# Optimization experiments

Hardware: AMD Instinct MI355X
Metric: run time of the kernel (lower is better)

## Reference

```python
import jax, jax.numpy as jnp
import numpy as np

K_ACTIVE = 32
MULTI_K = 64
AUX_K = 64
DEAD_THRESH = 256


def setup_inputs() -> dict:
    key = jax.random.key(0)
    ks = jax.random.split(key, 4)
    B, D, M = 4096, 1024, 16384
    x = jax.random.normal(ks[0], (B, D), dtype=jnp.float32)
    enc_w = jax.random.normal(ks[1], (M, D), dtype=jnp.float32) / np.sqrt(D)
    dec_w = jax.random.normal(ks[2], (D, M), dtype=jnp.float32) / np.sqrt(M)
    input_bias = jnp.zeros((D,), dtype=jnp.float32)
    neuron_bias = jnp.zeros((M,), dtype=jnp.float32)
    steps = jax.random.randint(ks[3], (M,), 0, 512).astype(jnp.int64)
    return {"x": x, "enc_w": enc_w, "dec_w": dec_w,
            "input_bias": input_bias, "neuron_bias": neuron_bias, "steps": steps}


def reference(x, enc_w, dec_w, input_bias, neuron_bias, steps):
    # encode: center, linear (no bias), add neuron bias, relu
    x_cent = x - input_bias                                   # [B, D]
    pre_act = x_cent @ enc_w.T + neuron_bias                  # [B, M]
    acts = jax.nn.relu(pre_act)
    B, M = acts.shape

    # training path: global batch-wide top-(K*B) across flattened activations
    flat = acts.reshape(-1)                                   # [B*M]
    topk_vals, topk_idx = jax.lax.top_k(flat, K_ACTIVE * B)
    activ = jnp.zeros_like(flat).at[topk_idx].set(topk_vals).reshape(B, M)

    # multi-k branch: per-row top-k on pre-activations, relu, scatter, decode
    mvals, midx = jax.lax.top_k(pre_act, MULTI_K)             # [B, MULTI_K]
    mvals = jax.nn.relu(mvals)
    rows = jnp.arange(B)[:, None]
    multik_activ = jnp.zeros_like(pre_act).at[rows, midx].set(mvals)
    multik_recon = multik_activ @ dec_w.T + input_bias        # [B, D]

    # main reconstruction
    recon = activ @ dec_w.T + input_bias                      # [B, D]

    # dead-neuron bookkeeping + aux top-k over dead neurons
    steps = steps + 1
    active = activ.sum(axis=0) > 0                            # [M]
    steps = jnp.where(active, jnp.zeros_like(steps), steps)
    dead_mask = (steps > DEAD_THRESH).astype(pre_act.dtype)   # [M]
    dead_pre = pre_act * dead_mask                            # [B, M]
    aux_vals, aux_idx = jax.lax.top_k(dead_pre, AUX_K)        # [B, AUX_K]
    aux_vals = jax.nn.relu(aux_vals)

    return recon, activ, multik_recon, aux_vals, aux_idx
```

## Files before the change

### kernel.cpp

```cpp
#include <hip/hip_runtime.h>

#define K_ACTIVE 32
#define MULTI_K 64
#define AUX_K 64
#define DEAD_THRESH 256
#define BUF_CAP 262144u
#define SORT_CAP 4096

typedef unsigned int u32;
typedef unsigned long long u64;
typedef unsigned short ushort_t;
typedef __bf16 bf16x8 __attribute__((ext_vector_type(8)));
typedef float f32x4 __attribute__((ext_vector_type(4)));

__device__ __forceinline__ u32 fmap_signed_bits(u32 u) {
  return (u & 0x80000000u) ? ~u : (u | 0x80000000u);
}

__device__ __forceinline__ u32 bf16_rne(float f) {
  u32 u = __float_as_uint(f);
  return (u + 0x7FFFu + ((u >> 16) & 1u)) >> 16;
}

__device__ __forceinline__ void gload16(const void* g, void* s) {
  __builtin_amdgcn_global_load_lds(
      (const __attribute__((address_space(1))) void*)g,
      (__attribute__((address_space(3))) void*)s, 16, 0, 0);
}

__global__ void transpose_k(const float* __restrict__ in, float* __restrict__ out, int D, int M) {
  __shared__ float tile[32][33];
  const int bx = blockIdx.x * 32;
  const int by = blockIdx.y * 32;
  const int tx = threadIdx.x, ty = threadIdx.y;
  #pragma unroll
  for (int i = 0; i < 32; i += 8)
    tile[ty + i][tx] = in[(size_t)(by + ty + i) * M + bx + tx];
  __syncthreads();
  #pragma unroll
  for (int i = 0; i < 32; i += 8)
    out[(size_t)(bx + ty + i) * D + by + tx] = tile[tx][ty + i];
}

__global__ void convA_k(const float* __restrict__ X, const float* __restrict__ IB,
                        ushort_t* __restrict__ AH, ushort_t* __restrict__ AL, int D) {
  const int idx = blockIdx.x * 256 + threadIdx.x;
  const int row = idx >> 7;
  const int dpos = (idx & 127) << 3;
  const float4* xr = reinterpret_cast<const float4*>(X + (size_t)row * D + dpos);
  const float4* br = reinterpret_cast<const float4*>(IB + dpos);
  float4 x0 = xr[0], x1 = xr[1], b0 = br[0], b1 = br[1];
  float c[8] = {x0.x - b0.x, x0.y - b0.y, x0.z - b0.z, x0.w - b0.w,
                x1.x - b1.x, x1.y - b1.y, x1.z - b1.z, x1.w - b1.w};
  u32 hw[4], lw[4];
  #pragma unroll
  for (int j = 0; j < 4; ++j) {
    u32 h0 = bf16_rne(c[2 * j]), h1 = bf16_rne(c[2 * j + 1]);
    float r0 = c[2 * j] - __uint_as_float(h0 << 16);
    float r1 = c[2 * j + 1] - __uint_as_float(h1 << 16);
    hw[j] = h0 | (h1 << 16);
    lw[j] = bf16_rne(r0) | (bf16_rne(r1) << 16);
  }
  reinterpret_cast<uint4*>(AH)[idx] = make_uint4(hw[0], hw[1], hw[2], hw[3]);
  reinterpret_cast<uint4*>(AL)[idx] = make_uint4(lw[0], lw[1], lw[2], lw[3]);
}

__global__ void convW_k(const float* __restrict__ W,
                        ushort_t* __restrict__ WH, ushort_t* __restrict__ WL) {
  const int idx = blockIdx.x * 256 + threadIdx.x;
  const float4* wr = reinterpret_cast<const float4*>(W) + (size_t)idx * 2;
  float4 x0 = wr[0], x1 = wr[1];
  float c[8] = {x0.x, x0.y, x0.z, x0.w, x1.x, x1.y, x1.z, x1.w};
  u32 hw[4], lw[4];
  #pragma unroll
  for (int j = 0; j < 4; ++j) {
    u32 h0 = bf16_rne(c[2 * j]), h1 = bf16_rne(c[2 * j + 1]);
    float r0 = c[2 * j] - __uint_as_float(h0 << 16);
    float r1 = c[2 * j + 1] - __uint_as_float(h1 << 16);
    hw[j] = h0 | (h1 << 16);
    lw[j] = bf16_rne(r0) | (bf16_rne(r1) << 16);
  }
  reinterpret_cast<uint4*>(WH)[idx] = make_uint4(hw[0], hw[1], hw[2], hw[3]);
  reinterpret_cast<uint4*>(WL)[idx] = make_uint4(lw[0], lw[1], lw[2], lw[3]);
}

__global__ __launch_bounds__(256) void gemm_mfma(
    const ushort_t* __restrict__ AH, const ushort_t* __restrict__ AL,
    const ushort_t* __restrict__ WH, const ushort_t* __restrict__ WL,
    const float* __restrict__ NB, float* __restrict__ OUT,
    u32* __restrict__ GH, int M) {
  extern __shared__ char smem[];
  ushort_t* sA = (ushort_t*)smem;
  ushort_t* sB = (ushort_t*)(smem + 16384);
  const int tid = threadIdx.x;
  const int wave = tid >> 6, lane = tid & 63;
  const int bm = blockIdx.y * 128, bn = blockIdx.x * 128;
  const int wm = wave & 1, wn = wave >> 1;

  f32x4 acc[4][4];
  #pragma unroll
  for (int i = 0; i < 4; ++i)
    #pragma unroll
    for (int j = 0; j < 4; ++j) acc[i][j] = (f32x4){0.f, 0.f, 0.f, 0.f};

  int rowA[4], cbS[4];
  #pragma unroll
  for (int r = 0; r < 4; ++r) {
    int o = ((wave << 2) + r) * 1024 + lane * 16;
    int row = o >> 7;
    int cb = o & 127;
    rowA[r] = row;
    cbS[r] = cb ^ ((row & 7) << 4);
  }
  const int cl = lane & 15, kg = lane >> 4;

  for (int kt = 0; kt < 48; ++kt) {
    const int ph = kt >> 4;
    const size_t kb = (size_t)((kt & 15) << 6) * 2;
    const ushort_t* Asrc = (ph == 1) ? AL : AH;
    const ushort_t* Bsrc = (ph == 2) ? WL : WH;
    #pragma unroll
    for (int r = 0; r < 4; ++r) {
      gload16((const char*)Asrc + ((size_t)(bm + rowA[r]) * 2048 + kb + cbS[r]),
              (char*)sA + (((wave << 2) + r) << 10));
      gload16((const char*)Bsrc + ((size_t)(bn + rowA[r]) * 2048 + kb + cbS[r]),
              (char*)sB + (((wave << 2) + r) << 10));
    }
    __syncthreads();
    #pragma unroll
    for (int ks = 0; ks < 2; ++ks) {
      const int kbyte = ks * 64 + kg * 16;
      bf16x8 af[4], bfr[4];
      #pragma unroll
      for (int mi = 0; mi < 4; ++mi) {
        const int rA = wm * 64 + mi * 16 + cl;
        af[mi] = *reinterpret_cast<const bf16x8*>(
            (const char*)sA + rA * 128 + (kbyte ^ ((rA & 7) << 4)));
      }
      #pragma unroll
      for (int ni = 0; ni < 4; ++ni) {
        const int rB = wn * 64 + ni * 16 + cl;
        bfr[ni] = *reinterpret_cast<const bf16x8*>(
            (const char*)sB + rB * 128 + (kbyte ^ ((rB & 7) << 4)));
      }
      #pragma unroll
      for (int mi = 0; mi < 4; ++mi)
        #pragma unroll
        for (int ni = 0; ni < 4; ++ni)
          acc[mi][ni] = __builtin_amdgcn_mfma_f32_16x16x32_bf16(af[mi], bfr[ni], acc[mi][ni], 0, 0, 0);
    }
    __syncthreads();
  }

  u32* eh = (u32*)smem;
  for (int i = tid; i < 8192; i += 256) eh[i] = 0;
  __syncthreads();
  const int rg = lane >> 4;
  const int rb = (lane & 3) * 2048;
  #pragma unroll
  for (int ni = 0; ni < 4; ++ni) {
    const int col = bn + wn * 64 + ni * 16 + cl;
    const float nbv = NB[col];
    #pragma unroll
    for (int mi = 0; mi < 4; ++mi) {
      const int row0 = bm + wm * 64 + mi * 16 + rg * 4;
      #pragma unroll
      for (int r = 0; r < 4; ++r) {
        const float val = acc[mi][ni][r] + nbv;
        OUT[(size_t)(row0 + r) * M + col] = val;
        const float a = (val > 0.f) ? val : 0.f;
        atomicAdd(&eh[rb + (__float_as_uint(a) >> 21)], 1u);
      }
    }
  }
  __syncthreads();
  for (int i = tid; i < 2048; i += 256) {
    u32 s = eh[i] + eh[2048 + i] + eh[4096 + i] + eh[6144 + i];
    if (s) atomicAdd(&GH[i], s);
  }
}

__global__ void scan_k(const u32* __restrict__ H, u32* __restrict__ PRM, u32 K, int phase) {
  __shared__ u32 suf[256];
  const int t = threadIdx.x;
  u32 h[8], ls[8];
  #pragma unroll
  for (int j = 0; j < 8; ++j) h[j] = H[t * 8 + j];
  u32 run = 0;
  #pragma unroll
  for (int j = 7; j >= 0; --j) { run += h[j]; ls[j] = run; }
  suf[t] = run;
  __syncthreads();
  for (int off = 1; off < 256; off <<= 1) {
    u32 v = (t + off < 256) ? suf[t + off] : 0u;
    __syncthreads();
    suf[t] += v;
    __syncthreads();
  }
  const u32 rightOf = (t < 255) ? suf[t + 1] : 0u;
  const u32 base = (phase == 2) ? PRM[1] : 0u;
  #pragma unroll
  for (int j = 0; j < 8; ++j) {
    u32 Sb = base + rightOf + ls[j];
    u32 Sb1 = base + rightOf + ((j < 7) ? ls[j + 1] : 0u);
    if (Sb >= K && Sb1 < K) {
      int b = t * 8 + j;
      if (phase == 1) { PRM[0] = (u32)b; PRM[1] = Sb1; }
      else { PRM[2] = (PRM[0] << 11) | (u32)b; PRM[3] = K - Sb1; }
    }
  }
}

__global__ void hist2_k(const float4* __restrict__ P4, size_t N4, const u32* __restrict__ PRM, u32* __restrict__ GH) {
  const u32 b1 = PRM[0];
  const size_t step = (size_t)gridDim.x * blockDim.x;
  for (size_t i = (size_t)blockIdx.x * blockDim.x + threadIdx.x; i < N4; i += step) {
    float4 vv = P4[i];
    float va[4] = {vv.x, vv.y, vv.z, vv.w};
    #pragma unroll
    for (int c = 0; c < 4; ++c) {
      float a = (va[c] > 0.f) ? va[c] : 0.f;
      u32 u = __float_as_uint(a);
      if ((u >> 21) == b1) atomicAdd(&GH[(u >> 10) & 2047u], 1u);
    }
  }
}

__global__ void collect_k(const float4* __restrict__ P4, size_t N4, u32* __restrict__ PRM,
                          float* __restrict__ BV, u32* __restrict__ BI,
                          u32* __restrict__ CF, int M) {
  const u32 pc = PRM[2];
  const size_t step = (size_t)gridDim.x * blockDim.x;
  for (size_t i = (size_t)blockIdx.x * blockDim.x + threadIdx.x; i < N4; i += step) {
    float4 vv = P4[i];
    float va[4] = {vv.x, vv.y, vv.z, vv.w};
    #pragma unroll
    for (int c = 0; c < 4; ++c) {
      float a = (va[c] > 0.f) ? va[c] : 0.f;
      u32 u = __float_as_uint(a);
      u32 bin = u >> 10;
      if (bin == pc) {
        u32 pos = atomicAdd(&PRM[8], 1u);
        if (pos < BUF_CAP) { BV[pos] = a; BI[pos] = (u32)(i * 4 + c); }
      } else if (bin > pc) {
        if (a > 0.f) CF[(u32)((i * 4 + c) % (size_t)M)] = 1u;
      }
    }
  }
}

__global__ void sortmark_k(u32* __restrict__ PRM, const float* __restrict__ BV, const u32* __restrict__ BI,
                           float* __restrict__ SV, u32* __restrict__ SI, u32* __restrict__ CF, int M) {
  __shared__ u64 keys[SORT_CAP];
  const int tid = threadIdx.x;
  u32 nb = PRM[8]; if (nb > SORT_CAP) nb = SORT_CAP;
  const u32 krem = PRM[3];
  if (nb == 0) { if (tid == 0) PRM[5] = 0; return; }
  u32 np = 1; while (np < nb) np <<= 1;
  for (u32 i = tid; i < np; i += 256)
    keys[i] = (i < nb) ? ((((u64)__float_as_uint(BV[i])) << 32) | (u64)(0xFFFFFFFFu - BI[i])) : 0ull;
  __syncthreads();
  for (u32 k = 2; k <= np; k <<= 1) {
    for (u32 j = k >> 1; j > 0; j >>= 1) {
      for (u32 i = tid; i < np; i += 256) {
        u32 ixj = i ^ j;
        if (ixj > i) {
          u64 a = keys[i], b = keys[ixj];
          bool up = ((i & k) == 0);
          if (up ? (a < b) : (a > b)) { keys[i] = b; keys[ixj] = a; }
        }
      }
      __syncthreads();
    }
  }
  u32 nsel = krem < nb ? krem : nb;
  for (u32 t = tid; t < nsel; t += 256) {
    u64 kk = keys[t];
    u32 flat = 0xFFFFFFFFu - (u32)(kk & 0xFFFFFFFFull);
    float val = __uint_as_float((u32)(kk >> 32));
    SI[t] = flat; SV[t] = val;
    if (val > 0.f) CF[flat % (u32)M] = 1u;
  }
  if (tid == 0) PRM[5] = nsel;
}

__global__ void dead_k(const u32* __restrict__ CF, const int* __restrict__ ST,
                       u32* __restrict__ DW, int M) {
  int w = blockIdx.x * blockDim.x + threadIdx.x;
  if (w >= M / 32) return;
  u32 bits = 0;
  for (int i = 0; i < 32; ++i) {
    int n = w * 32 + i;
    if (CF[n] == 0 && (ST[n] + 1) > DEAD_THRESH) bits |= (1u << i);
  }
  DW[w] = bits;
}

struct TopkSh {
  u32 hist[16 * 257];
  u32 wred[4];
  u32 prefix, need, scnt;
  int selN[64];
  float selV[64];
};

template<bool ZSKIP>
__device__ void row_topk64(const float (&v)[64], int tid, TopkSh* S) {
  const int lane = tid & 63, wid = tid >> 6;
  u32 zp = 0, zn = 0;
  if (ZSKIP) {
    #pragma unroll
    for (int j = 0; j < 64; ++j) {
      u32 ub = __float_as_uint(v[j]);
      zp += (ub == 0u);
      zn += (ub == 0x80000000u);
    }
    #pragma unroll
    for (int o = 32; o > 0; o >>= 1) { zp += __shfl_down(zp, o); zn += __shfl_down(zn, o); }
  }
  u32 pref = 0, need = 64;
  for (int p = 0; p < 4; ++p) {
    const int sh = 24 - 8 * p;
    for (int i = tid; i < 16 * 257; i += 256) S->hist[i] = 0;
    if (p == 0 && tid == 0) S->scnt = 0;
    __syncthreads();
    const int rb = (tid & 15) * 257;
    #pragma unroll
    for (int j = 0; j < 64; ++j) {
      u32 ub = __float_as_uint(v[j]);
      if (ZSKIP && ((ub << 1) == 0u)) continue;
      u32 mu = fmap_signed_bits(ub);
      if (p == 0 || (mu >> (sh + 8)) == pref)
        atomicAdd(&S->hist[rb + ((mu >> sh) & 255u)], 1u);
    }
    if (ZSKIP && lane == 0) {
      const u32 mup = 0x80000000u, mun = 0x7FFFFFFFu;
      if (zp && (p == 0 || (mup >> (sh + 8)) == pref))
        atomicAdd(&S->hist[wid * 257 + ((mup >> sh) & 255u)], zp);
      if (zn && (p == 0 || (mun >> (sh + 8)) == pref))
        atomicAdd(&S->hist[wid * 257 + ((mun >> sh) & 255u)], zn);
    }
    __syncthreads();
    u32 own = 0;
    #pragma unroll
    for (int r = 0; r < 16; ++r) own += S->hist[r * 257 + tid];
    u32 x = own;
    #pragma unroll
    for (int o = 1; o < 64; o <<= 1) {
      u32 y = __shfl_down(x, o);
      x += (lane + o < 64) ? y : 0u;
    }
    if (lane == 0) S->wred[wid] = x;
    __syncthreads();
    u32 Sb = x;
    for (int w = wid + 1; w < 4; ++w) Sb += S->wred[w];
    u32 below = Sb - own;
    if (Sb >= need && below < need) {
      S->prefix = (pref << 8) | (u32)tid;
      S->need = need - below;
    }
    __syncthreads();
    pref = S->prefix; need = S->need;
  }
  const u32 muc = pref, neq = need;
  u32 myeq = 0;
  #pragma unroll
  for (int j = 0; j < 64; ++j) {
    u32 mu = fmap_signed_bits(__float_as_uint(v[j]));
    if (mu > muc) {
      u32 pos = atomicAdd(&S->scnt, 1u);
      S->selN[pos] = tid * 64 + j;
      S->selV[pos] = v[j];
    } else if (mu == muc) ++myeq;
  }
  u32 xs = myeq;
  #pragma unroll
  for (int o = 1; o < 64; o <<= 1) {
    u32 y = __shfl_up(xs, o);
    xs += (lane >= o) ? y : 0u;
  }
  if (lane == 63) S->wred[wid] = xs;
  __syncthreads();
  u32 base = 0;
  for (int w = 0; w < wid; ++w) base += S->wred[w];
  u32 g = base + xs - myeq;
  const u32 a0 = S->scnt;
  #pragma unroll
  for (int j = 0; j < 64; ++j) {
    u32 mu = fmap_signed_bits(__float_as_uint(v[j]));
    if (mu == muc) {
      if (g < neq) { S->selN[a0 + g] = tid * 64 + j; S->selV[a0 + g] = v[j]; }
      ++g;
    }
  }
  __syncthreads();
}

__device__ __forceinline__ void load_row64(const float* rowp, float (&v)[64]) {
  #pragma unroll
  for (int j = 0; j < 16; ++j) {
    float4 t = reinterpret_cast<const float4*>(rowp)[j];
    v[4 * j + 0] = t.x; v[4 * j + 1] = t.y; v[4 * j + 2] = t.z; v[4 * j + 3] = t.w;
  }
}

__launch_bounds__(256, 2)
__global__ void rowk_multik(const float* __restrict__ PRE, const float* __restrict__ WT,
                            const float* __restrict__ IB, float* __restrict__ MR,
                            int M, int D) {
  __shared__ TopkSh S;
  const int b = blockIdx.x, tid = threadIdx.x;
  float v[64];
  load_row64(PRE + (size_t)b * M + tid * 64, v);
  row_topk64<false>(v, tid, &S);
  const int d0 = tid * 4;
  float4 acc = *reinterpret_cast<const float4*>(IB + d0);
  for (int i = 0; i < 64; ++i) {
    float w = S.selV[i];
    if (w > 0.f) {
      const float4 wv = *reinterpret_cast<const float4*>(WT + (size_t)S.selN[i] * D + d0);
      acc.x = fmaf(w, wv.x, acc.x); acc.y = fmaf(w, wv.y, acc.y);
      acc.z = fmaf(w, wv.z, acc.z); acc.w = fmaf(w, wv.w, acc.w);
    }
  }
  *reinterpret_cast<float4*>(MR + (size_t)b * D + d0) = acc;
}

__launch_bounds__(256, 2)
__global__ void rowk_aux(const float* __restrict__ PRE, const u32* __restrict__ DW,
                         float* __restrict__ AV, float* __restrict__ AI, int M) {
  __shared__ TopkSh S;
  __shared__ u64 skey[64];
  __shared__ int sN2[64];
  __shared__ float sV2[64];
  const int b = blockIdx.x, tid = threadIdx.x;
  float v[64];
  load_row64(PRE + (size_t)b * M + tid * 64, v);
  const u32 mw0 = DW[tid * 2], mw1 = DW[tid * 2 + 1];
  #pragma unroll
  for (int j = 0; j < 64; ++j) {
    u32 bit = ((j < 32 ? mw0 : mw1) >> (j & 31)) & 1u;
    v[j] = bit ? v[j] : (v[j] * 0.0f);
  }
  row_topk64<true>(v, tid, &S);
  if (tid < 64) {
    float vv = S.selV[tid];
    int col = S.selN[tid];
    u32 mu = fmap_signed_bits(__float_as_uint(vv));
    skey[tid] = (((u64)mu) << 32) | (u64)(0xFFFFFFFFu - (u32)col);
  }
  __syncthreads();
  if (tid < 64) {
    u64 mine = skey[tid];
    int rank = 0;
    for (int j = 0; j < 64; ++j) rank += (skey[j] > mine) ? 1 : 0;
    sN2[rank] = S.selN[tid]; sV2[rank] = S.selV[tid];
  }
  __syncthreads();
  if (tid < 64) {
    AV[(size_t)b * AUX_K + tid] = sV2[tid] > 0.f ? sV2[tid] : 0.f;
    AI[(size_t)b * AUX_K + tid] = (float)sN2[tid];
  }
}

__launch_bounds__(256, 2)
__global__ void rowk_scatter(float* __restrict__ ACT, const float* __restrict__ WT,
                             const float* __restrict__ IB, float* __restrict__ RC,
                             const u32* __restrict__ PRM, const float* __restrict__ SV,
                             const u32* __restrict__ SI, int M, int D) {
  __shared__ int lsN[2048]; __shared__ float lsV[2048];
  __shared__ int ovN[256]; __shared__ float ovV[256];
  __shared__ u32 ovc, lc;
  const int b = blockIdx.x, tid = threadIdx.x;
  float* rowp = ACT + (size_t)b * M + tid * 64;
  float v[64];
  load_row64(rowp, v);
  const u32 pc = PRM[2];
  #pragma unroll
  for (int j = 0; j < 64; ++j) {
    float a = (v[j] > 0.f) ? v[j] : 0.f;
    v[j] = ((__float_as_uint(a) >> 10) > pc) ? a : 0.f;
  }
  if (tid == 0) ovc = 0;
  __syncthreads();
  const u32 nbs = PRM[5];
  for (u32 t = tid; t < nbs; t += 256) {
    u32 flat = SI[t];
    if (flat / (u32)M == (u32)b) {
      u32 p = atomicAdd(&ovc, 1u);
      if (p < 256) { ovN[p] = (int)(flat % (u32)M); ovV[p] = SV[t]; }
    }
  }
  __syncthreads();
  const u32 no = ovc < 256u ? ovc : 256u;
  #pragma unroll
  for (int j = 0; j < 64; ++j) {
    const int col = tid * 64 + j;
    for (u32 i = 0; i < no; ++i) if (ovN[i] == col) v[j] = ovV[i];
  }
  #pragma unroll
  for (int j = 0; j < 16; ++j) {
    float4 t = make_float4(v[4 * j + 0], v[4 * j + 1], v[4 * j + 2], v[4 * j + 3]);
    reinterpret_cast<float4*>(rowp)[j] = t;
  }
  const int d0 = tid * 4;
  float4 acc = *reinterpret_cast<const float4*>(IB + d0);
  for (int cpart = 0; cpart < 8; ++cpart) {
    if (tid == 0) lc = 0;
    __syncthreads();
    if ((tid >> 5) == cpart) {
      #pragma unroll
      for (int j = 0; j < 64; ++j) {
        if (v[j] > 0.f) {
          u32 p = atomicAdd(&lc, 1u);
          lsN[p] = tid * 64 + j; lsV[p] = v[j];
        }
      }
    }
    __syncthreads();
    const u32 n = lc;
    for (u32 i = 0; i < n; ++i) {
      const float w = lsV[i];
      const float4 wv = *reinterpret_cast<const float4*>(WT + (size_t)lsN[i] * D + d0);
      acc.x = fmaf(w, wv.x, acc.x); acc.y = fmaf(w, wv.y, acc.y);
      acc.z = fmaf(w, wv.z, acc.z); acc.w = fmaf(w, wv.w, acc.w);
    }
    __syncthreads();
  }
  *reinterpret_cast<float4*>(RC + (size_t)b * D + d0) = acc;
}

extern "C" void kernel_launch(void* const* d_in, const int* in_sizes, int n_in,
                              void* d_out, int out_size, void* d_ws, size_t ws_size,
                              hipStream_t stream) {
  const float* x  = (const float*)d_in[0];
  const float* ew = (const float*)d_in[1];
  const float* dw = (const float*)d_in[2];
  const float* ib = (const float*)d_in[3];
  const float* nb = (const float*)d_in[4];
  const int* steps = (const int*)d_in[5];
  const int D = in_sizes[3];
  const int M = in_sizes[4];
  const int B = in_sizes[0] / D;
  const u32 K = (u32)(K_ACTIVE * B);

  float* out = (float*)d_out;
  float* recon  = out;
  float* activ  = out + (size_t)B * D;
  float* mrecon = activ + (size_t)B * M;
  float* avals  = mrecon + (size_t)B * D;
  float* aidx   = avals + (size_t)B * AUX_K;

  ushort_t* AH = (ushort_t*)recon;
  ushort_t* AL = (ushort_t*)mrecon;

  char* wsp = (char*)d_ws;
  size_t o = 0;
  auto alloc = [&](size_t bytes) { char* p = wsp + o; o += (bytes + 255) & ~(size_t)255; return p; };
  ushort_t* WH = (ushort_t*)alloc((size_t)M * D * 2);
  ushort_t* WL = (ushort_t*)alloc((size_t)M * D * 2);
  float* WT = (float*)alloc((size_t)M * D * 4);
  u32* H1   = (u32*)alloc(8192);
  u32* H2   = (u32*)alloc(8192);
  u32* PRM  = (u32*)alloc(256);
  u32* CF   = (u32*)alloc((size_t)M * 4);
  u32* DW   = (u32*)alloc((size_t)(M / 32) * 4);
  float* BV = (float*)alloc((size_t)BUF_CAP * 4);
  u32* BI   = (u32*)alloc((size_t)BUF_CAP * 4);
  float* SV = (float*)alloc((size_t)SORT_CAP * 4);
  u32* SI   = (u32*)alloc((size_t)SORT_CAP * 4);
  (void)ws_size; (void)n_in; (void)out_size;

  hipMemsetAsync(H1, 0, 8192, stream);
  hipMemsetAsync(H2, 0, 8192, stream);
  hipMemsetAsync(PRM, 0, 256, stream);
  hipMemsetAsync(CF, 0, (size_t)M * 4, stream);

  convA_k<<<(B * D / 8 + 255) / 256, 256, 0, stream>>>(x, ib, AH, AL, D);
  convW_k<<<((size_t)M * D / 8 + 255) / 256, 256, 0, stream>>>(ew, WH, WL);
  transpose_k<<<dim3(M / 32, D / 32), dim3(32, 8), 0, stream>>>(dw, WT, D, M);
  gemm_mfma<<<dim3(M / 128, B / 128), 256, 32768, stream>>>(AH, AL, WH, WL, nb, activ, H1, M);

  const size_t N4 = (size_t)B * M / 4;
  const float4* act4 = (const float4*)activ;
  scan_k<<<1, 256, 0, stream>>>(H1, PRM, K, 1);
  hist2_k<<<2048, 256, 0, stream>>>(act4, N4, PRM, H2);
  scan_k<<<1, 256, 0, stream>>>(H2, PRM, K, 2);
  collect_k<<<2048, 256, 0, stream>>>(act4, N4, PRM, BV, BI, CF, M);
  sortmark_k<<<1, 256, 0, stream>>>(PRM, BV, BI, SV, SI, CF, M);
  dead_k<<<(M / 32 + 255) / 256, 256, 0, stream>>>(CF, steps, DW, M);
  rowk_multik<<<B, 256, 0, stream>>>(activ, WT, ib, mrecon, M, D);
  rowk_aux<<<B, 256, 0, stream>>>(activ, DW, avals, aidx, M);
  rowk_scatter<<<B, 256, 0, stream>>>(activ, WT, ib, recon, PRM, SV, SI, M, D);
}
```

Before: 1.500 ms.

## Drop the second full activation pass by staging candidates during histogram pass

The second histogram pass now also stages every element of the first-level bin into a global buffer, through per-block shared-memory staging. A small collect2 kernel then filters that buffer for the final bin, which removes the full 256MB collect pass. Neuron activity for elements above the threshold is now taken from a per-column max that the GEMM epilogue records with atomicMax. The GEMM grid is also remapped to a 1D grid with a swizzled block order, which may change L2 locality. The risks are a larger candidate buffer that can overflow, and extra atomics in the GEMM epilogue.

```diff
diff --git a/kernel.cpp b/kernel.cpp
--- a/kernel.cpp
+++ b/kernel.cpp
@@ -4,7 +4,8 @@
 #define MULTI_K 64
 #define AUX_K 64
 #define DEAD_THRESH 256
-#define BUF_CAP 262144u
+#define BUF_CAP 2097152u
+#define STG_CAP 4096
 #define SORT_CAP 4096
 
 typedef unsigned int u32;
@@ -88,13 +89,18 @@
     const ushort_t* __restrict__ AH, const ushort_t* __restrict__ AL,
     const ushort_t* __restrict__ WH, const ushort_t* __restrict__ WL,
     const float* __restrict__ NB, float* __restrict__ OUT,
-    u32* __restrict__ GH, int M) {
+    u32* __restrict__ GH, u32* __restrict__ CM, int M, int B) {
   extern __shared__ char smem[];
   ushort_t* sA = (ushort_t*)smem;
   ushort_t* sB = (ushort_t*)(smem + 16384);
   const int tid = threadIdx.x;
   const int wave = tid >> 6, lane = tid & 63;
-  const int bm = blockIdx.y * 128, bn = blockIdx.x * 128;
+  const int nbx = M >> 7;
+  const int nwg = (B >> 7) * nbx;
+  const int cpx = nwg >> 3;
+  const int bid = blockIdx.x;
+  const int wg = (bid & 7) * cpx + (bid >> 3);
+  const int bm = (wg / nbx) << 7, bn = (wg % nbx) << 7;
   const int wm = wave & 1, wn = wave >> 1;
 
   f32x4 acc[4][4];
@@ -161,6 +167,7 @@
   for (int ni = 0; ni < 4; ++ni) {
     const int col = bn + wn * 64 + ni * 16 + cl;
     const float nbv = NB[col];
+    float mx = 0.f;
     #pragma unroll
     for (int mi = 0; mi < 4; ++mi) {
       const int row0 = bm + wm * 64 + mi * 16 + rg * 4;
@@ -169,9 +176,13 @@
         const float val = acc[mi][ni][r] + nbv;
         OUT[(size_t)(row0 + r) * M + col] = val;
         const float a = (val > 0.f) ? val : 0.f;
+        mx = fmaxf(mx, a);
         atomicAdd(&eh[rb + (__float_as_uint(a) >> 21)], 1u);
       }
     }
+    mx = fmaxf(mx, __shfl_xor(mx, 16));
+    mx = fmaxf(mx, __shfl_xor(mx, 32));
+    if (rg == 0) atomicMax(&CM[col], __float_as_uint(mx));
   }
   __syncthreads();
   for (int i = tid; i < 2048; i += 256) {
@@ -211,40 +222,56 @@
   }
 }
 
-__global__ void hist2_k(const float4* __restrict__ P4, size_t N4, const u32* __restrict__ PRM, u32* __restrict__ GH) {
+__global__ void hist2_k(const float4* __restrict__ P4, size_t N4, u32* __restrict__ PRM,
+                        u32* __restrict__ GH, float* __restrict__ BV, u32* __restrict__ BI) {
+  __shared__ float sv[STG_CAP];
+  __shared__ u32 si[STG_CAP];
+  __shared__ u32 scnt, sbase;
+  const int tid = threadIdx.x;
+  if (tid == 0) scnt = 0;
+  __syncthreads();
   const u32 b1 = PRM[0];
   const size_t step = (size_t)gridDim.x * blockDim.x;
-  for (size_t i = (size_t)blockIdx.x * blockDim.x + threadIdx.x; i < N4; i += step) {
+  for (size_t i = (size_t)blockIdx.x * blockDim.x + tid; i < N4; i += step) {
     float4 vv = P4[i];
     float va[4] = {vv.x, vv.y, vv.z, vv.w};
     #pragma unroll
     for (int c = 0; c < 4; ++c) {
       float a = (va[c] > 0.f) ? va[c] : 0.f;
       u32 u = __float_as_uint(a);
-      if ((u >> 21) == b1) atomicAdd(&GH[(u >> 10) & 2047u], 1u);
-    }
-  }
-}
-
-__global__ void collect_k(const float4* __restrict__ P4, size_t N4, u32* __restrict__ PRM,
-                          float* __restrict__ BV, u32* __restrict__ BI,
-                          u32* __restrict__ CF, int M) {
+      if ((u >> 21) == b1) {
+        atomicAdd(&GH[(u >> 10) & 2047u], 1u);
+        u32 p = atomicAdd(&scnt, 1u);
+        if (p < STG_CAP) { sv[p] = a; si[p] = (u32)(i * 4 + c); }
+        else {
+          u32 g = atomicAdd(&PRM[8], 1u);
+          if (g < BUF_CAP) { BV[g] = a; BI[g] = (u32)(i * 4 + c); }
+        }
+      }
+    }
+  }
+  __syncthreads();
+  u32 n = scnt < STG_CAP ? scnt : STG_CAP;
+  if (tid == 0) sbase = atomicAdd(&PRM[8], n);
+  __syncthreads();
+  const u32 base = sbase;
+  for (u32 i = tid; i < n; i += 256) {
+    u32 g = base + i;
+    if (g < BUF_CAP) { BV[g] = sv[i]; BI[g] = si[i]; }
+  }
+}
+
+__global__ void collect2_k(u32* __restrict__ PRM, const float* __restrict__ BV,
+                           const u32* __restrict__ BI, float* __restrict__ BV2,
+                           u32* __restrict__ BI2) {
   const u32 pc = PRM[2];
-  const size_t step = (size_t)gridDim.x * blockDim.x;
-  for (size_t i = (size_t)blockIdx.x * blockDim.x + threadIdx.x; i < N4; i += step) {
-    float4 vv = P4[i];
-    float va[4] = {vv.x, vv.y, vv.z, vv.w};
-    #pragma unroll
-    for (int c = 0; c < 4; ++c) {
-      float a = (va[c] > 0.f) ? va[c] : 0.f;
-      u32 u = __float_as_uint(a);
-      u32 bin = u >> 10;
-      if (bin == pc) {
-        u32 pos = atomicAdd(&PRM[8], 1u);
-        if (pos < BUF_CAP) { BV[pos] = a; BI[pos] = (u32)(i * 4 + c); }
-      } else if (bin > pc) {
-        if (a > 0.f) CF[(u32)((i * 4 + c) % (size_t)M)] = 1u;
-      }
+  u32 nb1 = PRM[8]; if (nb1 > BUF_CAP) nb1 = BUF_CAP;
+  const u32 step = gridDim.x * blockDim.x;
+  for (u32 i = blockIdx.x * blockDim.x + threadIdx.x; i < nb1; i += step) {
+    float a = BV[i];
+    if ((__float_as_uint(a) >> 10) == pc) {
+      u32 pos = atomicAdd(&PRM[9], 1u);
+      if (pos < SORT_CAP) { BV2[pos] = a; BI2[pos] = BI[i]; }
     }
   }
 }
@@ -253,7 +280,7 @@
                            float* __restrict__ SV, u32* __restrict__ SI, u32* __restrict__ CF, int M) {
   __shared__ u64 keys[SORT_CAP];
   const int tid = threadIdx.x;
-  u32 nb = PRM[8]; if (nb > SORT_CAP) nb = SORT_CAP;
+  u32 nb = PRM[9]; if (nb > SORT_CAP) nb = SORT_CAP;
   const u32 krem = PRM[3];
   if (nb == 0) { if (tid == 0) PRM[5] = 0; return; }
   u32 np = 1; while (np < nb) np <<= 1;
@@ -284,14 +311,17 @@
   if (tid == 0) PRM[5] = nsel;
 }
 
-__global__ void dead_k(const u32* __restrict__ CF, const int* __restrict__ ST,
+__global__ void dead_k(const u32* __restrict__ CF, const u32* __restrict__ CM,
+                       const int* __restrict__ ST, const u32* __restrict__ PRM,
                        u32* __restrict__ DW, int M) {
   int w = blockIdx.x * blockDim.x + threadIdx.x;
   if (w >= M / 32) return;
+  const u32 pc = PRM[2];
   u32 bits = 0;
   for (int i = 0; i < 32; ++i) {
     int n = w * 32 + i;
-    if (CF[n] == 0 && (ST[n] + 1) > DEAD_THRESH) bits |= (1u << i);
+    bool active = (CF[n] != 0) || ((CM[n] >> 10) > pc);
+    if (!active && (ST[n] + 1) > DEAD_THRESH) bits |= (1u << i);
   }
   DW[w] = bits;
 }
@@ -564,9 +594,12 @@
   u32* H2   = (u32*)alloc(8192);
   u32* PRM  = (u32*)alloc(256);
   u32* CF   = (u32*)alloc((size_t)M * 4);
+  u32* CM   = (u32*)alloc((size_t)M * 4);
   u32* DW   = (u32*)alloc((size_t)(M / 32) * 4);
   float* BV = (float*)alloc((size_t)BUF_CAP * 4);
   u32* BI   = (u32*)alloc((size_t)BUF_CAP * 4);
+  float* BV2 = (float*)alloc((size_t)SORT_CAP * 4);
+  u32* BI2   = (u32*)alloc((size_t)SORT_CAP * 4);
   float* SV = (float*)alloc((size_t)SORT_CAP * 4);
   u32* SI   = (u32*)alloc((size_t)SORT_CAP * 4);
   (void)ws_size; (void)n_in; (void)out_size;
@@ -575,20 +608,22 @@
   hipMemsetAsync(H2, 0, 8192, stream);
   hipMemsetAsync(PRM, 0, 256, stream);
   hipMemsetAsync(CF, 0, (size_t)M * 4, stream);
+  hipMemsetAsync(CM, 0, (size_t)M * 4, stream);
 
   convA_k<<<(B * D / 8 + 255) / 256, 256, 0, stream>>>(x, ib, AH, AL, D);
   convW_k<<<((size_t)M * D / 8 + 255) / 256, 256, 0, stream>>>(ew, WH, WL);
   transpose_k<<<dim3(M / 32, D / 32), dim3(32, 8), 0, stream>>>(dw, WT, D, M);
-  gemm_mfma<<<dim3(M / 128, B / 128), 256, 32768, stream>>>(AH, AL, WH, WL, nb, activ, H1, M);
+  const int nwg = (B / 128) * (M / 128);
+  gemm_mfma<<<nwg, 256, 32768, stream>>>(AH, AL, WH, WL, nb, activ, H1, CM, M, B);
 
   const size_t N4 = (size_t)B * M / 4;
   const float4* act4 = (const float4*)activ;
   scan_k<<<1, 256, 0, stream>>>(H1, PRM, K, 1);
-  hist2_k<<<2048, 256, 0, stream>>>(act4, N4, PRM, H2);
+  hist2_k<<<2048, 256, 0, stream>>>(act4, N4, PRM, H2, BV, BI);
   scan_k<<<1, 256, 0, stream>>>(H2, PRM, K, 2);
-  collect_k<<<2048, 256, 0, stream>>>(act4, N4, PRM, BV, BI, CF, M);
-  sortmark_k<<<1, 256, 0, stream>>>(PRM, BV, BI, SV, SI, CF, M);
-  dead_k<<<(M / 32 + 255) / 256, 256, 0, stream>>>(CF, steps, DW, M);
+  collect2_k<<<64, 256, 0, stream>>>(PRM, BV, BI, BV2, BI2);
+  sortmark_k<<<1, 256, 0, stream>>>(PRM, BV2, BI2, SV, SI, CF, M);
+  dead_k<<<(M / 32 + 255) / 256, 256, 0, stream>>>(CF, CM, steps, PRM, DW, M);
   rowk_multik<<<B, 256, 0, stream>>>(activ, WT, ib, mrecon, M, D);
   rowk_aux<<<B, 256, 0, stream>>>(activ, DW, avals, aidx, M);
   rowk_scatter<<<B, 256, 0, stream>>>(activ, WT, ib, recon, PRM, SV, SI, M, D);
```

Result: faster. 1.469 ms (-2.1%).
